# Kernel optimization log

Hardware: AMD Instinct MI355X
Metric: run time of the kernel (lower is better)

## Reference

```python
import jax, jax.numpy as jnp
import numpy as np

N, S, Z, H, K, DEG = 8192, 4, 64, 128, 4, 16
E = N * DEG


def setup_inputs() -> dict:
    key = jax.random.key(0)
    ks = jax.random.split(key, 9)
    g = lambda k, shape, scale=1.0: jax.random.normal(k, shape, dtype=jnp.float32) * scale
    return dict(
        zIG=g(ks[0], (N, S, Z)),                         # node intention features
        xt_enc=g(ks[1], (N, S, H)),                      # encoded actions per node
        Ws=g(ks[2], (K, H, Z), 1.0 / np.sqrt(Z)),        # attn_s[k] weights (no bias)
        Wd=g(ks[3], (K, H, Z), 1.0 / np.sqrt(Z)),        # attn_d[k] weights
        F2_w1=g(ks[4], (H, 2 * H), 1.0 / np.sqrt(2 * H)),
        F2_w2=g(ks[5], (H, H), 1.0 / np.sqrt(H)),
        F1_w1=g(ks[6], (H, K * H), 1.0 / np.sqrt(K * H)),
        F1_w2=g(ks[7], (H, H), 1.0 / np.sqrt(H)),
        src=jax.random.randint(ks[8], (E,), 0, N),       # random source per edge
        dst=jnp.repeat(jnp.arange(N), DEG),              # regular graph: DEG in-edges per node, grouped
    )


def reference(zIG, xt_enc, Ws, Wd, F2_w1, F2_w2, F1_w1, F1_w2, src, dst):
    n, s, h = xt_enc.shape
    k = Ws.shape[0]
    deg = src.shape[0] // n

    # ---- edge_attention: eIG[e,s,k] = leaky_relu(sum_h (Ws_k z_src)*(Wd_k z_dst)) ----
    zs, zd = zIG[src], zIG[dst]                          # [E,S,Z] irregular gathers
    scores = []
    for kk in range(k):                                  # k is small & structural
        a_s = zs @ Ws[kk].T                              # [E,S,H]
        a_d = zd @ Wd[kk].T                              # [E,S,H]
        scores.append(jax.nn.leaky_relu((a_s * a_d).sum(-1)))  # [E,S]
    eIG = jnp.stack(scores, axis=-1)                     # [E,S,K]

    # ---- message_func: dA = F2(cat(xt_src, xt_dst)) ----
    msg_in = jnp.concatenate([xt_enc[src], xt_enc[dst]], axis=-1)   # [E,S,2H]
    dA = jax.nn.relu(msg_in @ F2_w1.T) @ F2_w2.T                    # [E,S,H]

    # ---- reduce_func: softmax over neighbor mailbox (dim=1), weighted mean ----
    # dst is grouped with constant degree, so the DGL mailbox is a reshape.
    alpha = jax.nn.softmax(eIG.reshape(n, deg, s, k), axis=1)       # [N,D,S,K]
    mail = dA.reshape(n, deg, s, h)                                 # [N,D,S,H]
    res = jnp.einsum('ndsk,ndsh->nskh', alpha, mail) / deg          # mean over D
    res = res.reshape(n, s, k * h)                                  # cat over k (k-major)
    deltax = jax.nn.relu(res @ F1_w1.T) @ F1_w2.T                   # [N,S,H]
    return deltax, alpha
```

## Files before the change

### kernel.cpp

```cpp
#include <hip/hip_runtime.h>
#include <hip/hip_bf16.h>

typedef unsigned short u16;
typedef unsigned int u32;
using ushort8 = __attribute__((ext_vector_type(8))) unsigned short;
using short8  = __attribute__((ext_vector_type(8))) short;
using f32x4   = __attribute__((ext_vector_type(4))) float;

__device__ __forceinline__ float bf2f(u16 v) {
  union { u32 u; float f; } x; x.u = ((u32)v) << 16; return x.f;
}
__device__ __forceinline__ float u2f(u32 u) {
  union { u32 u; float f; } x; x.u = u; return x.f;
}
__device__ __forceinline__ u16 f2bf(float f) {
  union { u32 u; float f; } x; x.f = f;
  u32 r = x.u + 0x7FFFu + ((x.u >> 16) & 1u);
  return (u16)(r >> 16);
}
__device__ __forceinline__ u32 pack2bf(float lo, float hi) {
  return (u32)f2bf(lo) | ((u32)f2bf(hi) << 16);
}
__device__ __forceinline__ float dot4(float4 a, float4 b) {
  return a.x * b.x + a.y * b.y + a.z * b.z + a.w * b.w;
}
__device__ __forceinline__ void stage_w(const float* g, int stride, int c, u16* Wl, int t) {
  int row = t >> 1, half = t & 1;
  const float4* gp = (const float4*)(g + (size_t)row * stride + c * 64 + half * 32);
  ushort8* d = (ushort8*)(Wl + row * 72 + half * 32);
  #pragma unroll
  for (int i = 0; i < 4; ++i) {
    float4 a = gp[2 * i], b = gp[2 * i + 1];
    ushort8 o;
    o[0] = f2bf(a.x); o[1] = f2bf(a.y); o[2] = f2bf(a.z); o[3] = f2bf(a.w);
    o[4] = f2bf(b.x); o[5] = f2bf(b.y); o[6] = f2bf(b.z); o[7] = f2bf(b.w);
    d[i] = o;
  }
}

__global__ __launch_bounds__(256) void k_prep(const float* __restrict__ Ws,
                                              const float* __restrict__ Wd,
                                              const float* __restrict__ F1w1,
                                              const float* __restrict__ F2w2,
                                              float* __restrict__ MT,
                                              float* __restrict__ WW2) {
  if (blockIdx.x < 64) {
    int t = blockIdx.x * 256 + threadIdx.x;
    int k = t >> 12, z2 = (t >> 6) & 63, z1 = t & 63;
    const float* wsp = Ws + k * 8192 + z1;
    const float* wdp = Wd + k * 8192 + z2;
    float acc = 0.f;
    #pragma unroll 8
    for (int h = 0; h < 128; ++h) acc += wsp[h * 64] * wdp[h * 64];
    MT[k * 4096 + z2 * 64 + z1] = acc;
  } else {
    int id = (blockIdx.x - 64) * 256 + threadIdx.x;
    int ho = id >> 9, kk = (id >> 7) & 3, hi = id & 127;
    const float* wa = F1w1 + ho * 512 + kk * 128;
    const float* wb = F2w2 + hi;
    float acc = 0.f;
    #pragma unroll 8
    for (int j = 0; j < 128; ++j) acc += wa[j] * wb[j * 128];
    WW2[ho * 512 + kk * 128 + hi] = acc * 0.0625f;
  }
}

__global__ __launch_bounds__(256) void k_stage2(const float* __restrict__ zIG,
                                                const float* __restrict__ MT,
                                                const float* __restrict__ xt,
                                                const float* __restrict__ W1,
                                                float* __restrict__ td,
                                                u16* __restrict__ u, u16* __restrict__ v) {
  __shared__ __align__(16) char smem[36864];
  int t = threadIdx.x;
  if (blockIdx.x < 1024) {
    float* zf = (float*)smem;
    int nb0 = blockIdx.x * 8;
    {
      const float4* zsrc = (const float4*)(zIG + (size_t)nb0 * 256);
      float4* zd = (float4*)zf;
      zd[t] = zsrc[t];
      zd[t + 256] = zsrc[t + 256];
    }
    __syncthreads();
    int s = t >> 6, k = (t >> 4) & 3, z1q = t & 15;
    const float4* mt4 = (const float4*)MT;
    float4 acc[8];
    #pragma unroll
    for (int g = 0; g < 8; ++g) acc[g] = make_float4(0.f, 0.f, 0.f, 0.f);
    for (int z2 = 0; z2 < 64; ++z2) {
      float4 mv = mt4[k * 1024 + z2 * 16 + z1q];
      #pragma unroll
      for (int g = 0; g < 8; ++g) {
        float zv = zf[g * 256 + s * 64 + z2];
        acc[g].x += mv.x * zv; acc[g].y += mv.y * zv;
        acc[g].z += mv.z * zv; acc[g].w += mv.w * zv;
      }
    }
    int sk = s * 4 + k;
    #pragma unroll
    for (int g = 0; g < 8; ++g)
      *(float4*)&td[(size_t)(nb0 + g) * 1024 + sk * 64 + z1q * 4] = acc[g];
  } else {
    u16* Wlu = (u16*)smem;
    u16* Wlv = (u16*)(smem + 18432);
    int lane = t & 63, w = t >> 6;
    size_t rowbase = (size_t)(blockIdx.x - 1024) * 128 + w * 32;
    int l15 = lane & 15, kc = lane >> 4;
    f32x4 au[2][8], av[2][8];
    #pragma unroll
    for (int mt = 0; mt < 2; ++mt)
      #pragma unroll
      for (int nt = 0; nt < 8; ++nt) {
        au[mt][nt] = (f32x4){0.f, 0.f, 0.f, 0.f};
        av[mt][nt] = (f32x4){0.f, 0.f, 0.f, 0.f};
      }
    for (int c = 0; c < 2; ++c) {
      __syncthreads();
      stage_w(W1,       256, c, Wlu, t);
      stage_w(W1 + 128, 256, c, Wlv, t);
      __syncthreads();
      #pragma unroll
      for (int ks = 0; ks < 2; ++ks) {
        short8 af[2];
        #pragma unroll
        for (int mt = 0; mt < 2; ++mt) {
          const float* ap = xt + (rowbase + mt * 16 + l15) * 128 + c * 64 + ks * 32 + kc * 8;
          float4 a0 = *(const float4*)ap, a1 = *(const float4*)(ap + 4);
          u16 tmp[8] = {f2bf(a0.x), f2bf(a0.y), f2bf(a0.z), f2bf(a0.w),
                        f2bf(a1.x), f2bf(a1.y), f2bf(a1.z), f2bf(a1.w)};
          af[mt] = *(short8*)tmp;
        }
        #pragma unroll
        for (int nt = 0; nt < 8; ++nt) {
          short8 bu = *(const short8*)&Wlu[(nt * 16 + l15) * 72 + ks * 32 + kc * 8];
          short8 bv = *(const short8*)&Wlv[(nt * 16 + l15) * 72 + ks * 32 + kc * 8];
          #pragma unroll
          for (int mt = 0; mt < 2; ++mt) {
            au[mt][nt] = __builtin_amdgcn_mfma_f32_16x16x32_bf16(af[mt], bu, au[mt][nt], 0, 0, 0);
            av[mt][nt] = __builtin_amdgcn_mfma_f32_16x16x32_bf16(af[mt], bv, av[mt][nt], 0, 0, 0);
          }
        }
      }
    }
    #pragma unroll
    for (int mt = 0; mt < 2; ++mt)
      #pragma unroll
      for (int nt = 0; nt < 8; ++nt)
        #pragma unroll
        for (int j = 0; j < 4; ++j) {
          size_t idx = (rowbase + mt * 16 + kc * 4 + j) * 128 + nt * 16 + l15;
          u[idx] = f2bf(au[mt][nt][j]);
          v[idx] = f2bf(av[mt][nt][j]);
        }
  }
}

__global__ __launch_bounds__(256) void k_score(
    const float* __restrict__ zIG, const int* __restrict__ src,
    const float* __restrict__ td, const u16* __restrict__ uW, const u16* __restrict__ vW,
    float* __restrict__ out, u16* __restrict__ m_ws) {
  __shared__ int srcIdx[16];
  __shared__ float tds[16 * 68];
  __shared__ float s17[16 * 17];
  __shared__ float e17[16 * 17];
  __shared__ float a20[16 * 20];

  int t = threadIdx.x, n = blockIdx.x;
  if (t < 16) srcIdx[t] = src[n * 16 + t];
  {
    int r = t >> 4, cc = t & 15;
    *(float4*)&tds[r * 68 + cc * 4] = ((const float4*)(td + (size_t)n * 1024))[r * 16 + cc];
  }
  __syncthreads();
  {
    int d = t >> 4, s = (t >> 2) & 3, k = t & 3;
    int sn = srcIdx[d];
    const float4* zp = (const float4*)(zIG + (size_t)sn * 256 + s * 64);
    int base = s * 4;
    float p0 = 0.f, p1 = 0.f, p2 = 0.f, p3 = 0.f;
    #pragma unroll
    for (int i = 0; i < 4; ++i) {
      float4 zv = zp[i * 4 + k];
      int o = i * 16 + k * 4;
      p0 += dot4(zv, *(const float4*)&tds[(base + 0) * 68 + o]);
      p1 += dot4(zv, *(const float4*)&tds[(base + 1) * 68 + o]);
      p2 += dot4(zv, *(const float4*)&tds[(base + 2) * 68 + o]);
      p3 += dot4(zv, *(const float4*)&tds[(base + 3) * 68 + o]);
    }
    p0 += __shfl_xor(p0, 1); p1 += __shfl_xor(p1, 1);
    p2 += __shfl_xor(p2, 1); p3 += __shfl_xor(p3, 1);
    p0 += __shfl_xor(p0, 2); p1 += __shfl_xor(p1, 2);
    p2 += __shfl_xor(p2, 2); p3 += __shfl_xor(p3, 2);
    float acc = (k == 0) ? p0 : (k == 1) ? p1 : (k == 2) ? p2 : p3;
    s17[d * 17 + base + k] = acc > 0.f ? acc : 0.01f * acc;
  }
  __syncthreads();
  float e_own;
  int dC = t >> 4, skC = t & 15;
  {
    float mx = -3.4e38f;
    #pragma unroll
    for (int dd = 0; dd < 16; ++dd) mx = fmaxf(mx, s17[dd * 17 + skC]);
    e_own = __expf(s17[dC * 17 + skC] - mx);
    e17[dC * 17 + skC] = e_own;
  }
  __syncthreads();
  {
    float sum = 0.f;
    #pragma unroll
    for (int dd = 0; dd < 16; ++dd) sum += e17[dd * 17 + skC];
    float a = e_own / sum;
    a20[dC * 20 + skC] = a;
    out[4194304u + (unsigned)n * 256 + t] = a;
  }
  __syncthreads();
  {
    int hp = t & 63, s = t >> 6;
    u32 vbits = *(const u32*)(vW + (size_t)n * 512 + s * 128 + hp * 2);
    float v_lo = u2f(vbits << 16), v_hi = u2f(vbits & 0xffff0000u);
    const u32* up = (const u32*)uW;
    float m0l = 0.f, m0h = 0.f, m1l = 0.f, m1h = 0.f;
    float m2l = 0.f, m2h = 0.f, m3l = 0.f, m3h = 0.f;
    for (int d = 0; d < 16; ++d) {
      int sn = srcIdx[d];
      u32 ub = up[(size_t)sn * 256 + s * 64 + hp];
      float r_lo = fmaxf(u2f(ub << 16) + v_lo, 0.f);
      float r_hi = fmaxf(u2f(ub & 0xffff0000u) + v_hi, 0.f);
      float4 a = *(const float4*)&a20[d * 20 + s * 4];
      m0l += a.x * r_lo; m0h += a.x * r_hi;
      m1l += a.y * r_lo; m1h += a.y * r_hi;
      m2l += a.z * r_lo; m2h += a.z * r_hi;
      m3l += a.w * r_lo; m3h += a.w * r_hi;
    }
    u32* mp = (u32*)(m_ws + (size_t)n * 2048);
    mp[(s * 4 + 0) * 64 + hp] = pack2bf(m0l, m0h);
    mp[(s * 4 + 1) * 64 + hp] = pack2bf(m1l, m1h);
    mp[(s * 4 + 2) * 64 + hp] = pack2bf(m2l, m2h);
    mp[(s * 4 + 3) * 64 + hp] = pack2bf(m3l, m3h);
  }
}

__global__ __launch_bounds__(256) void k_fg(const u16* __restrict__ A,
                                            const float* __restrict__ WF,
                                            const float* __restrict__ WG,
                                            float* __restrict__ out) {
  __shared__ u16 Wl[128 * 72];
  __shared__ u16 hidl[128 * 136];
  int t = threadIdx.x, lane = t & 63, w = t >> 6;
  size_t rowbase = (size_t)blockIdx.x * 128 + w * 32;
  int l15 = lane & 15, kc = lane >> 4;
  f32x4 acc[2][8];
  #pragma unroll
  for (int mt = 0; mt < 2; ++mt)
    #pragma unroll
    for (int nt = 0; nt < 8; ++nt) acc[mt][nt] = (f32x4){0.f, 0.f, 0.f, 0.f};
  for (int c = 0; c < 8; ++c) {
    __syncthreads();
    stage_w(WF, 512, c, Wl, t);
    __syncthreads();
    #pragma unroll
    for (int ks = 0; ks < 2; ++ks) {
      short8 af[2];
      #pragma unroll
      for (int mt = 0; mt < 2; ++mt)
        af[mt] = *(const short8*)(A + (rowbase + mt * 16 + l15) * 512 + c * 64 + ks * 32 + kc * 8);
      #pragma unroll
      for (int nt = 0; nt < 8; ++nt) {
        short8 bf = *(const short8*)&Wl[(nt * 16 + l15) * 72 + ks * 32 + kc * 8];
        #pragma unroll
        for (int mt = 0; mt < 2; ++mt)
          acc[mt][nt] = __builtin_amdgcn_mfma_f32_16x16x32_bf16(af[mt], bf, acc[mt][nt], 0, 0, 0);
      }
    }
  }
  #pragma unroll
  for (int mt = 0; mt < 2; ++mt)
    #pragma unroll
    for (int nt = 0; nt < 8; ++nt)
      #pragma unroll
      for (int j = 0; j < 4; ++j)
        hidl[(w * 32 + mt * 16 + kc * 4 + j) * 136 + nt * 16 + l15] =
            f2bf(fmaxf(acc[mt][nt][j], 0.f));
  f32x4 acc2[2][8];
  #pragma unroll
  for (int mt = 0; mt < 2; ++mt)
    #pragma unroll
    for (int nt = 0; nt < 8; ++nt) acc2[mt][nt] = (f32x4){0.f, 0.f, 0.f, 0.f};
  for (int c = 0; c < 2; ++c) {
    __syncthreads();
    stage_w(WG, 128, c, Wl, t);
    __syncthreads();
    #pragma unroll
    for (int ks = 0; ks < 2; ++ks) {
      short8 af[2];
      #pragma unroll
      for (int mt = 0; mt < 2; ++mt)
        af[mt] = *(const short8*)&hidl[(w * 32 + mt * 16 + l15) * 136 + c * 64 + ks * 32 + kc * 8];
      #pragma unroll
      for (int nt = 0; nt < 8; ++nt) {
        short8 bf = *(const short8*)&Wl[(nt * 16 + l15) * 72 + ks * 32 + kc * 8];
        #pragma unroll
        for (int mt = 0; mt < 2; ++mt)
          acc2[mt][nt] = __builtin_amdgcn_mfma_f32_16x16x32_bf16(af[mt], bf, acc2[mt][nt], 0, 0, 0);
      }
    }
  }
  #pragma unroll
  for (int mt = 0; mt < 2; ++mt)
    #pragma unroll
    for (int nt = 0; nt < 8; ++nt)
      #pragma unroll
      for (int j = 0; j < 4; ++j)
        out[(rowbase + mt * 16 + kc * 4 + j) * 128 + nt * 16 + l15] = acc2[mt][nt][j];
}

extern "C" void kernel_launch(void* const* d_in, const int* in_sizes, int n_in,
                              void* d_out, int out_size, void* d_ws, size_t ws_size,
                              hipStream_t stream) {
  const float* zIG  = (const float*)d_in[0];
  const float* xt   = (const float*)d_in[1];
  const float* Ws   = (const float*)d_in[2];
  const float* Wd   = (const float*)d_in[3];
  const float* F2w1 = (const float*)d_in[4];
  const float* F2w2 = (const float*)d_in[5];
  const float* F1w1 = (const float*)d_in[6];
  const float* F1w2 = (const float*)d_in[7];
  const int* src    = (const int*)d_in[8];
  float* out = (float*)d_out;

  char* ws = (char*)d_ws;
  float* MT  = (float*)ws;
  float* td  = (float*)(ws + 65536);
  u16* u     = (u16*)(ws + 65536 + 33554432);
  u16* v     = u + 4194304;
  float* WW2 = (float*)(ws + 50397184);
  u16* m     = (u16*)(ws + 50659328);

  k_prep  <<<320,  256, 0, stream>>>(Ws, Wd, F1w1, F2w2, MT, WW2);
  k_stage2<<<1280, 256, 0, stream>>>(zIG, MT, xt, F2w1, td, u, v);
  k_score <<<8192, 256, 0, stream>>>(zIG, src, td, u, v, out, m);
  k_fg    <<<256,  256, 0, stream>>>(m, WW2, F1w2, out);
}
```

Baseline: 117.8 us.

## Compute td projection with split-bf16 MFMA and split stage2 into two kernels

The zIG·M^T bilinear projection moves from a scalar FP32 FMA loop to MFMA bf16 instructions. Precision is kept with a hi/lo bf16 split (three MFMAs per tile), and k_prep now emits the matrix as hi/lo bf16 halves. The combined stage2 kernel is split into a separate k_td (512 blocks) and k_uv (256 blocks) launch. The aim is to remove the VALU-bound td computation, at the cost of an extra kernel launch and a small precision change from the 3-term split.

```diff
diff --git a/kernel.cpp b/kernel.cpp
--- a/kernel.cpp
+++ b/kernel.cpp
@@ -23,6 +23,18 @@
 }
 __device__ __forceinline__ float dot4(float4 a, float4 b) {
   return a.x * b.x + a.y * b.y + a.z * b.z + a.w * b.w;
+}
+__device__ __forceinline__ void split8(const float* ap, short8& hi, short8& lo) {
+  float4 a0 = *(const float4*)ap, a1 = *(const float4*)(ap + 4);
+  float e[8] = {a0.x, a0.y, a0.z, a0.w, a1.x, a1.y, a1.z, a1.w};
+  u16 h[8], l[8];
+  #pragma unroll
+  for (int j = 0; j < 8; ++j) {
+    u32 b = __float_as_uint(e[j]);
+    h[j] = (u16)(b >> 16);
+    l[j] = f2bf(e[j] - u2f(b & 0xffff0000u));
+  }
+  hi = *(short8*)h; lo = *(short8*)l;
 }
 __device__ __forceinline__ void stage_w(const float* g, int stride, int c, u16* Wl, int t) {
   int row = t >> 1, half = t & 1;
@@ -42,17 +54,19 @@
                                               const float* __restrict__ Wd,
                                               const float* __restrict__ F1w1,
                                               const float* __restrict__ F2w2,
-                                              float* __restrict__ MT,
+                                              u16* __restrict__ Bh, u16* __restrict__ Bl,
                                               float* __restrict__ WW2) {
   if (blockIdx.x < 64) {
     int t = blockIdx.x * 256 + threadIdx.x;
-    int k = t >> 12, z2 = (t >> 6) & 63, z1 = t & 63;
+    int k = t >> 12, z1 = (t >> 6) & 63, z2 = t & 63;
     const float* wsp = Ws + k * 8192 + z1;
     const float* wdp = Wd + k * 8192 + z2;
     float acc = 0.f;
     #pragma unroll 8
     for (int h = 0; h < 128; ++h) acc += wsp[h * 64] * wdp[h * 64];
-    MT[k * 4096 + z2 * 64 + z1] = acc;
+    u32 b = __float_as_uint(acc);
+    Bh[(k * 64 + z1) * 64 + z2] = (u16)(b >> 16);
+    Bl[(k * 64 + z1) * 64 + z2] = f2bf(acc - u2f(b & 0xffff0000u));
   } else {
     int id = (blockIdx.x - 64) * 256 + threadIdx.x;
     int ho = id >> 9, kk = (id >> 7) & 3, hi = id & 127;
@@ -65,95 +79,114 @@
   }
 }
 
-__global__ __launch_bounds__(256) void k_stage2(const float* __restrict__ zIG,
-                                                const float* __restrict__ MT,
-                                                const float* __restrict__ xt,
-                                                const float* __restrict__ W1,
-                                                float* __restrict__ td,
-                                                u16* __restrict__ u, u16* __restrict__ v) {
-  __shared__ __align__(16) char smem[36864];
-  int t = threadIdx.x;
-  if (blockIdx.x < 1024) {
-    float* zf = (float*)smem;
-    int nb0 = blockIdx.x * 8;
-    {
-      const float4* zsrc = (const float4*)(zIG + (size_t)nb0 * 256);
-      float4* zd = (float4*)zf;
-      zd[t] = zsrc[t];
-      zd[t + 256] = zsrc[t + 256];
-    }
-    __syncthreads();
-    int s = t >> 6, k = (t >> 4) & 3, z1q = t & 15;
-    const float4* mt4 = (const float4*)MT;
-    float4 acc[8];
-    #pragma unroll
-    for (int g = 0; g < 8; ++g) acc[g] = make_float4(0.f, 0.f, 0.f, 0.f);
-    for (int z2 = 0; z2 < 64; ++z2) {
-      float4 mv = mt4[k * 1024 + z2 * 16 + z1q];
-      #pragma unroll
-      for (int g = 0; g < 8; ++g) {
-        float zv = zf[g * 256 + s * 64 + z2];
-        acc[g].x += mv.x * zv; acc[g].y += mv.y * zv;
-        acc[g].z += mv.z * zv; acc[g].w += mv.w * zv;
-      }
-    }
-    int sk = s * 4 + k;
-    #pragma unroll
-    for (int g = 0; g < 8; ++g)
-      *(float4*)&td[(size_t)(nb0 + g) * 1024 + sk * 64 + z1q * 4] = acc[g];
-  } else {
-    u16* Wlu = (u16*)smem;
-    u16* Wlv = (u16*)(smem + 18432);
-    int lane = t & 63, w = t >> 6;
-    size_t rowbase = (size_t)(blockIdx.x - 1024) * 128 + w * 32;
-    int l15 = lane & 15, kc = lane >> 4;
-    f32x4 au[2][8], av[2][8];
+__global__ __launch_bounds__(256) void k_td(const float* __restrict__ zIG,
+                                            const u16* __restrict__ Bh_g,
+                                            const u16* __restrict__ Bl_g,
+                                            float* __restrict__ td) {
+  __shared__ u16 Bh[128 * 72];
+  __shared__ u16 Bl[128 * 72];
+  int t = threadIdx.x, lane = t & 63, w = t >> 6;
+  int chalf = blockIdx.x & 1;
+  size_t rowbase = (size_t)(blockIdx.x >> 1) * 128 + w * 32;
+  {
+    int row = t >> 1, half = t & 1;
+    const ushort8* gh = (const ushort8*)(Bh_g + (chalf * 128 + row) * 64 + half * 32);
+    const ushort8* gl = (const ushort8*)(Bl_g + (chalf * 128 + row) * 64 + half * 32);
+    ushort8* dh = (ushort8*)(Bh + row * 72 + half * 32);
+    ushort8* dl = (ushort8*)(Bl + row * 72 + half * 32);
+    #pragma unroll
+    for (int i = 0; i < 4; ++i) { dh[i] = gh[i]; dl[i] = gl[i]; }
+  }
+  __syncthreads();
+  int l15 = lane & 15, kc = lane >> 4;
+  f32x4 acc[2][8];
+  #pragma unroll
+  for (int mt = 0; mt < 2; ++mt)
+    #pragma unroll
+    for (int nt = 0; nt < 8; ++nt) acc[mt][nt] = (f32x4){0.f, 0.f, 0.f, 0.f};
+  #pragma unroll
+  for (int ks = 0; ks < 2; ++ks) {
+    short8 ah[2], al[2];
     #pragma unroll
     for (int mt = 0; mt < 2; ++mt)
+      split8(zIG + (rowbase + mt * 16 + l15) * 64 + ks * 32 + kc * 8, ah[mt], al[mt]);
+    #pragma unroll
+    for (int nt = 0; nt < 8; ++nt) {
+      int bo = (nt * 16 + l15) * 72 + ks * 32 + kc * 8;
+      short8 bh = *(const short8*)&Bh[bo];
+      short8 bl = *(const short8*)&Bl[bo];
+      #pragma unroll
+      for (int mt = 0; mt < 2; ++mt) {
+        acc[mt][nt] = __builtin_amdgcn_mfma_f32_16x16x32_bf16(ah[mt], bh, acc[mt][nt], 0, 0, 0);
+        acc[mt][nt] = __builtin_amdgcn_mfma_f32_16x16x32_bf16(al[mt], bh, acc[mt][nt], 0, 0, 0);
+        acc[mt][nt] = __builtin_amdgcn_mfma_f32_16x16x32_bf16(ah[mt], bl, acc[mt][nt], 0, 0, 0);
+      }
+    }
+  }
+  #pragma unroll
+  for (int mt = 0; mt < 2; ++mt)
+    #pragma unroll
+    for (int nt = 0; nt < 8; ++nt)
+      #pragma unroll
+      for (int j = 0; j < 4; ++j)
+        td[(rowbase + mt * 16 + kc * 4 + j) * 256 + chalf * 128 + nt * 16 + l15] =
+            acc[mt][nt][j];
+}
+
+__global__ __launch_bounds__(256) void k_uv(const float* __restrict__ xt,
+                                            const float* __restrict__ W1,
+                                            u16* __restrict__ u, u16* __restrict__ v) {
+  __shared__ u16 Wlu[128 * 72];
+  __shared__ u16 Wlv[128 * 72];
+  int t = threadIdx.x, lane = t & 63, w = t >> 6;
+  size_t rowbase = (size_t)blockIdx.x * 128 + w * 32;
+  int l15 = lane & 15, kc = lane >> 4;
+  f32x4 au[2][8], av[2][8];
+  #pragma unroll
+  for (int mt = 0; mt < 2; ++mt)
+    #pragma unroll
+    for (int nt = 0; nt < 8; ++nt) {
+      au[mt][nt] = (f32x4){0.f, 0.f, 0.f, 0.f};
+      av[mt][nt] = (f32x4){0.f, 0.f, 0.f, 0.f};
+    }
+  for (int c = 0; c < 2; ++c) {
+    __syncthreads();
+    stage_w(W1,       256, c, Wlu, t);
+    stage_w(W1 + 128, 256, c, Wlv, t);
+    __syncthreads();
+    #pragma unroll
+    for (int ks = 0; ks < 2; ++ks) {
+      short8 af[2];
+      #pragma unroll
+      for (int mt = 0; mt < 2; ++mt) {
+        const float* ap = xt + (rowbase + mt * 16 + l15) * 128 + c * 64 + ks * 32 + kc * 8;
+        float4 a0 = *(const float4*)ap, a1 = *(const float4*)(ap + 4);
+        u16 tmp[8] = {f2bf(a0.x), f2bf(a0.y), f2bf(a0.z), f2bf(a0.w),
+                      f2bf(a1.x), f2bf(a1.y), f2bf(a1.z), f2bf(a1.w)};
+        af[mt] = *(short8*)tmp;
+      }
       #pragma unroll
       for (int nt = 0; nt < 8; ++nt) {
-        au[mt][nt] = (f32x4){0.f, 0.f, 0.f, 0.f};
-        av[mt][nt] = (f32x4){0.f, 0.f, 0.f, 0.f};
-      }
-    for (int c = 0; c < 2; ++c) {
-      __syncthreads();
-      stage_w(W1,       256, c, Wlu, t);
-      stage_w(W1 + 128, 256, c, Wlv, t);
-      __syncthreads();
-      #pragma unroll
-      for (int ks = 0; ks < 2; ++ks) {
-        short8 af[2];
+        short8 bu = *(const short8*)&Wlu[(nt * 16 + l15) * 72 + ks * 32 + kc * 8];
+        short8 bv = *(const short8*)&Wlv[(nt * 16 + l15) * 72 + ks * 32 + kc * 8];
         #pragma unroll
         for (int mt = 0; mt < 2; ++mt) {
-          const float* ap = xt + (rowbase + mt * 16 + l15) * 128 + c * 64 + ks * 32 + kc * 8;
-          float4 a0 = *(const float4*)ap, a1 = *(const float4*)(ap + 4);
-          u16 tmp[8] = {f2bf(a0.x), f2bf(a0.y), f2bf(a0.z), f2bf(a0.w),
-                        f2bf(a1.x), f2bf(a1.y), f2bf(a1.z), f2bf(a1.w)};
-          af[mt] = *(short8*)tmp;
+          au[mt][nt] = __builtin_amdgcn_mfma_f32_16x16x32_bf16(af[mt], bu, au[mt][nt], 0, 0, 0);
+          av[mt][nt] = __builtin_amdgcn_mfma_f32_16x16x32_bf16(af[mt], bv, av[mt][nt], 0, 0, 0);
         }
-        #pragma unroll
-        for (int nt = 0; nt < 8; ++nt) {
-          short8 bu = *(const short8*)&Wlu[(nt * 16 + l15) * 72 + ks * 32 + kc * 8];
-          short8 bv = *(const short8*)&Wlv[(nt * 16 + l15) * 72 + ks * 32 + kc * 8];
-          #pragma unroll
-          for (int mt = 0; mt < 2; ++mt) {
-            au[mt][nt] = __builtin_amdgcn_mfma_f32_16x16x32_bf16(af[mt], bu, au[mt][nt], 0, 0, 0);
-            av[mt][nt] = __builtin_amdgcn_mfma_f32_16x16x32_bf16(af[mt], bv, av[mt][nt], 0, 0, 0);
-          }
-        }
-      }
-    }
-    #pragma unroll
-    for (int mt = 0; mt < 2; ++mt)
-      #pragma unroll
-      for (int nt = 0; nt < 8; ++nt)
-        #pragma unroll
-        for (int j = 0; j < 4; ++j) {
-          size_t idx = (rowbase + mt * 16 + kc * 4 + j) * 128 + nt * 16 + l15;
-          u[idx] = f2bf(au[mt][nt][j]);
-          v[idx] = f2bf(av[mt][nt][j]);
-        }
-  }
+      }
+    }
+  }
+  #pragma unroll
+  for (int mt = 0; mt < 2; ++mt)
+    #pragma unroll
+    for (int nt = 0; nt < 8; ++nt)
+      #pragma unroll
+      for (int j = 0; j < 4; ++j) {
+        size_t idx = (rowbase + mt * 16 + kc * 4 + j) * 128 + nt * 16 + l15;
+        u[idx] = f2bf(au[mt][nt][j]);
+        v[idx] = f2bf(av[mt][nt][j]);
+      }
 }
 
 __global__ __launch_bounds__(256) void k_score(
@@ -330,15 +363,17 @@
   float* out = (float*)d_out;
 
   char* ws = (char*)d_ws;
-  float* MT  = (float*)ws;
+  u16* Bh    = (u16*)ws;
+  u16* Bl    = Bh + 16384;
   float* td  = (float*)(ws + 65536);
   u16* u     = (u16*)(ws + 65536 + 33554432);
   u16* v     = u + 4194304;
   float* WW2 = (float*)(ws + 50397184);
   u16* m     = (u16*)(ws + 50659328);
 
-  k_prep  <<<320,  256, 0, stream>>>(Ws, Wd, F1w1, F2w2, MT, WW2);
-  k_stage2<<<1280, 256, 0, stream>>>(zIG, MT, xt, F2w1, td, u, v);
-  k_score <<<8192, 256, 0, stream>>>(zIG, src, td, u, v, out, m);
-  k_fg    <<<256,  256, 0, stream>>>(m, WW2, F1w2, out);
-}
+  k_prep <<<320,  256, 0, stream>>>(Ws, Wd, F1w1, F2w2, Bh, Bl, WW2);
+  k_td   <<<512,  256, 0, stream>>>(zIG, Bh, Bl, td);
+  k_uv   <<<256,  256, 0, stream>>>(xt, F2w1, u, v);
+  k_score<<<8192, 256, 0, stream>>>(zIG, src, td, u, v, out, m);
+  k_fg   <<<256,  256, 0, stream>>>(m, WW2, F1w2, out);
+}
```

Result: faster. 106.2 us (-9.9%).
